# Optimization experiments

Measured on AMD Instinct MI355X. Metric: run time of the kernel, lower is better.

## Reference

```python
import jax, jax.numpy as jnp
import numpy as np

jax.config.update("jax_enable_x64", True)  # exact int64 fixed-point requantization

QMIN, QMAX = 0, 255  # 8-bit asymmetric activations


def _mul_m0_shift(acc, M0, shift):
    """gemmlowp-style fixed-point rescale: round((acc*M0)>>31) >> shift (rounding)."""
    prod = acc.astype(jnp.int64) * M0.astype(jnp.int64)
    nudge = jnp.where(prod >= 0, jnp.int64(1 << 30), jnp.int64(1 - (1 << 30)))
    hi = (prod + nudge) >> 31  # rounding-doubling high mul
    sh = shift.astype(jnp.int64)
    return (hi + (jnp.int64(1) << (sh - 1))) >> sh  # rounding right shift


def _requant(acc, M0, shift, z_out):
    return jnp.clip(_mul_m0_shift(acc, M0, shift) + z_out, QMIN, QMAX).astype(jnp.int32)


def _qconv(q, w, z_in, M0, shift, z_out, pad):
    # int8-style conv: subtract input zero-point, integer accumulate (exact in fp32
    # since |acc| < 2^24 by construction), then fixed-point requantize.
    xf = (q - z_in).astype(jnp.float32)
    acc = jax.lax.conv_general_dilated(
        xf, w, (1, 1), [(pad, pad), (pad, pad)],
        dimension_numbers=("NCHW", "OIHW", "NCHW"))
    return _requant(jnp.round(acc).astype(jnp.int64), M0, shift, z_out)


def _qbn(q, z_in, w, b, M0, shift, z_out):
    # fused quantized BN: per-channel integer affine + fixed-point requantize
    acc = (q.astype(jnp.int64) - z_in) * w.astype(jnp.int64)[None, :, None, None] \
          + b.astype(jnp.int64)[None, :, None, None]
    return _requant(acc, M0, shift, z_out)


def setup_inputs() -> dict:
    key = jax.random.key(0)
    ks = jax.random.split(key, 10)
    B, Cin, H, W = 32, 256, 56, 56
    width, Cout = 64, 256
    x = jax.random.randint(ks[0], (B, Cin, H, W), 0, 256, dtype=jnp.int32)
    w1 = jax.random.randint(ks[1], (width, Cin, 1, 1), -63, 64).astype(jnp.float32)
    w2 = jax.random.randint(ks[2], (width, width, 3, 3), -63, 64).astype(jnp.float32)
    w3 = jax.random.randint(ks[3], (Cout, width, 1, 1), -63, 64).astype(jnp.float32)
    bn1_w = jax.random.randint(ks[4], (width,), 100, 160).astype(jnp.float32)
    bn1_b = jax.random.randint(ks[5], (width,), -1000, 1000).astype(jnp.float32)
    bn2_w = jax.random.randint(ks[6], (width,), 100, 160).astype(jnp.float32)
    bn2_b = jax.random.randint(ks[7], (width,), -1000, 1000).astype(jnp.float32)
    bn3_w = jax.random.randint(ks[8], (Cout,), 100, 160).astype(jnp.float32)
    bn3_b = jax.random.randint(ks[9], (Cout,), -1000, 1000).astype(jnp.float32)
    conv_zin = jnp.array([128, 128, 128], jnp.int32)
    conv_m0 = jnp.array([1518500250] * 3, jnp.int32)
    conv_shift = jnp.array([9, 9, 9], jnp.int32)
    conv_zout = jnp.array([128, 128, 128], jnp.int32)
    bn_m0 = jnp.array([1073741824] * 3, jnp.int32)
    bn_shift = jnp.array([6, 6, 6], jnp.int32)
    bn_zout = jnp.array([128, 128, 128], jnp.int32)
    add_z = jnp.array([128, 128], jnp.int32)
    add_m0 = jnp.array([1073741824] * 2, jnp.int32)
    add_shift = jnp.array([1, 1], jnp.int32)
    add_zout = jnp.array(128, jnp.int32)
    return dict(x=x, w1=w1, w2=w2, w3=w3,
                bn1_w=bn1_w, bn1_b=bn1_b, bn2_w=bn2_w, bn2_b=bn2_b,
                bn3_w=bn3_w, bn3_b=bn3_b,
                conv_zin=conv_zin, conv_m0=conv_m0, conv_shift=conv_shift,
                conv_zout=conv_zout, bn_m0=bn_m0, bn_shift=bn_shift,
                bn_zout=bn_zout, add_z=add_z, add_m0=add_m0,
                add_shift=add_shift, add_zout=add_zout)


def reference(x, w1, w2, w3, bn1_w, bn1_b, bn2_w, bn2_b, bn3_w, bn3_b,
              conv_zin, conv_m0, conv_shift, conv_zout,
              bn_m0, bn_shift, bn_zout,
              add_z, add_m0, add_shift, add_zout):
    identity = x  # a_bit == target_bit -> rescale_matrix path skipped, conv_x = x
    out = _qconv(x, w1, conv_zin[0], conv_m0[0], conv_shift[0], conv_zout[0], 0)
    out = _qbn(out, conv_zout[0], bn1_w, bn1_b, bn_m0[0], bn_shift[0], bn_zout[0])
    out = _qconv(out, w2, conv_zin[1], conv_m0[1], conv_shift[1], conv_zout[1], 1)
    out = _qbn(out, conv_zout[1], bn2_w, bn2_b, bn_m0[1], bn_shift[1], bn_zout[1])
    out = _qconv(out, w3, conv_zin[2], conv_m0[2], conv_shift[2], conv_zout[2], 0)
    out = _qbn(out, conv_zout[2], bn3_w, bn3_b, bn_m0[2], bn_shift[2], bn_zout[2])
    # QuantizedAdd: rescale both branches to the output scale, add, clamp
    ra = _mul_m0_shift(identity.astype(jnp.int64) - add_z[0], add_m0[0], add_shift[0])
    rb = _mul_m0_shift(out.astype(jnp.int64) - add_z[1], add_m0[1], add_shift[1])
    return jnp.clip(ra + rb + add_zout, QMIN, QMAX).astype(jnp.int32)
```

## Files before the change

### kernel.cpp

```cpp
#include <hip/hip_runtime.h>


typedef int v4i __attribute__((ext_vector_type(4)));

#define BATCH 32
#define CIN 256
#define CMID 64
#define HW 3136
#define W56 56

#define T1_BYTES ((size_t)BATCH * HW * CMID)
#define WP_BYTES ((size_t)68 * 64 * 16)

__device__ __forceinline__ int requant_q(int acc, int M0, int shift, int zout) {
    long long prod = (long long)acc * (long long)M0;
    long long nudge = (prod >= 0) ? (1LL << 30) : (1LL - (1LL << 30));
    long long hi = (prod + nudge) >> 31;
    long long r = (hi + (1LL << (shift - 1))) >> shift;
    int v = (int)r + zout;
    return v < 0 ? 0 : (v > 255 ? 255 : v);
}

__device__ __forceinline__ long long mulshift_ll(long long v, int M0, int shift) {
    long long prod = v * (long long)M0;
    long long nudge = (prod >= 0) ? (1LL << 30) : (1LL - (1LL << 30));
    long long hi = (prod + nudge) >> 31;
    return (hi + (1LL << (shift - 1))) >> shift;
}

__device__ __forceinline__ v4i pack16f(const float* src, int stride) {
    v4i r;
#pragma unroll
    for (int d = 0; d < 4; ++d) {
        unsigned int u = 0;
#pragma unroll
        for (int by = 0; by < 4; ++by) {
            int v = (int)src[(d * 4 + by) * stride];
            u |= ((unsigned int)(v & 255)) << (8 * by);
        }
        r[d] = (int)u;
    }
    return r;
}

__global__ __launch_bounds__(256) void k_prep(
    const float* __restrict__ w1, const float* __restrict__ w2,
    const float* __restrict__ w3, v4i* __restrict__ wp)
{
    int id = blockIdx.x * 256 + threadIdx.x;
    int fid = id >> 6, lane = id & 63;
    if (fid >= 68) return;
    int col = lane & 15, ci0 = (lane >> 4) * 16;
    const float* src;
    int stride;
    if (fid < 16) {
        int wv = fid >> 2, ks = fid & 3;
        src = w1 + (size_t)(wv * 16 + col) * 256 + ks * 64 + ci0;
        stride = 1;
    } else if (fid < 52) {
        int i = fid - 16, wv = i / 9, t = i - wv * 9;
        src = w2 + ((size_t)(wv * 16 + col) * 64 + ci0) * 9 + t;
        stride = 9;
    } else {
        int s = fid - 52;
        src = w3 + (size_t)(s * 16 + col) * 64 + ci0;
        stride = 1;
    }
    wp[fid * 64 + lane] = pack16f(src, stride);
}

__global__ __launch_bounds__(256, 4) void k_conv1(
    const int* __restrict__ x, const v4i* __restrict__ wp1,
    const float* __restrict__ bn_w, const float* __restrict__ bn_b,
    const int* __restrict__ conv_zin, const int* __restrict__ conv_m0,
    const int* __restrict__ conv_shift, const int* __restrict__ conv_zout,
    const int* __restrict__ bn_m0, const int* __restrict__ bn_shift,
    const int* __restrict__ bn_zout, signed char* __restrict__ t1)
{
    __shared__ v4i sm[560];
    const int tid = threadIdx.x, lane = tid & 63, wv = tid >> 6;
    const int col = lane & 15, koff = lane >> 4;
    const int b = blockIdx.y;
    const int hw0 = blockIdx.x * 112;
    const int co0 = wv * 16;

    v4i a[4];
#pragma unroll
    for (int ks = 0; ks < 4; ++ks) a[ks] = wp1[(wv * 4 + ks) * 64 + lane];

    const int cg = tid & 7, q = tid >> 3;
    const bool act = q < 28;
    const int zin = conv_zin[0];
    const int* xbase = x + (size_t)b * CIN * HW + hw0 + 4 * q;

    v4i xa[8], xa2[8];
    if (act) {
#pragma unroll
        for (int j = 0; j < 8; ++j)
            xa[j] = *(const v4i*)(xbase + (size_t)(cg * 8 + j) * HW);
    }

    v4i acc[7];
#pragma unroll
    for (int i = 0; i < 7; ++i) acc[i] = (v4i){0, 0, 0, 0};

    unsigned long long* smu = (unsigned long long*)sm;
#pragma unroll
    for (int ks = 0; ks < 4; ++ks) {
        if (ks) __syncthreads();
        if (act) {
#pragma unroll
            for (int p = 0; p < 4; ++p) {
                unsigned int lo = 0, hi = 0;
#pragma unroll
                for (int j = 0; j < 4; ++j) {
                    lo |= ((unsigned int)((xa[j][p] - zin) & 255)) << (8 * j);
                    hi |= ((unsigned int)((xa[j + 4][p] - zin) & 255)) << (8 * j);
                }
                smu[(q * 4 + p) * 10 + cg] = ((unsigned long long)hi << 32) | lo;
            }
        }
        __syncthreads();
        if (ks < 3 && act) {
#pragma unroll
            for (int j = 0; j < 8; ++j)
                xa2[j] = *(const v4i*)(xbase + (size_t)((ks + 1) * 64 + cg * 8 + j) * HW);
        }
#pragma unroll
        for (int nt = 0; nt < 7; ++nt) {
            v4i bf = sm[(nt * 16 + col) * 5 + koff];
            acc[nt] = __builtin_amdgcn_mfma_i32_16x16x64_i8(a[ks], bf, acc[nt], 0, 0, 0);
        }
        if (ks < 3) {
#pragma unroll
            for (int j = 0; j < 8; ++j) xa[j] = xa2[j];
        }
    }

    const int cm0 = conv_m0[0], csh = conv_shift[0], czo = conv_zout[0];
    const int bm0 = bn_m0[0], bsh = bn_shift[0], bzo = bn_zout[0];
    const int zin2 = conv_zin[1];
    const int rowb = koff * 4;
    int bw[4], bb[4];
#pragma unroll
    for (int r = 0; r < 4; ++r) {
        bw[r] = (int)bn_w[co0 + rowb + r];
        bb[r] = (int)bn_b[co0 + rowb + r];
    }
#pragma unroll
    for (int nt = 0; nt < 7; ++nt) {
        int n = b * HW + hw0 + nt * 16 + col;
        unsigned int pkd = 0;
#pragma unroll
        for (int r = 0; r < 4; ++r) {
            int qv = requant_q(acc[nt][r], cm0, csh, czo);
            int a2 = (qv - czo) * bw[r] + bb[r];
            int q2 = requant_q(a2, bm0, bsh, bzo);
            pkd |= ((unsigned int)((q2 - zin2) & 255)) << (8 * r);
        }
        *(unsigned int*)(t1 + (size_t)n * 64 + co0 + rowb) = pkd;
    }
}

__global__ __launch_bounds__(256, 3) void k_conv23(
    const signed char* __restrict__ t1, const v4i* __restrict__ wp2,
    const v4i* __restrict__ wp3,
    const float* __restrict__ bn2_w, const float* __restrict__ bn2_b,
    const float* __restrict__ bn3_w, const float* __restrict__ bn3_b,
    const int* __restrict__ x,
    const int* __restrict__ conv_zin, const int* __restrict__ conv_m0,
    const int* __restrict__ conv_shift, const int* __restrict__ conv_zout,
    const int* __restrict__ bn_m0, const int* __restrict__ bn_shift,
    const int* __restrict__ bn_zout,
    const int* __restrict__ add_z, const int* __restrict__ add_m0,
    const int* __restrict__ add_shift, const int* __restrict__ add_zout,
    int* __restrict__ out)
{
    __shared__ v4i sm[1120];
    __shared__ v4i t2s[560];
    const int tid = threadIdx.x, lane = tid & 63, wv = tid >> 6;
    const int col = lane & 15, koff = lane >> 4;
    const int b = blockIdx.y;
    const int r0 = blockIdx.x * 2;
    const int co0 = wv * 16;
    const int rowb = koff * 4;

    v4i a[9];
#pragma unroll
    for (int t = 0; t < 9; ++t) a[t] = wp2[(wv * 9 + t) * 64 + lane];

    const v4i* t1v = (const v4i*)t1;
#pragma unroll
    for (int k = 0; k < 4; ++k) {
        int idx = tid + k * 256;
        if (idx < 896) {
            int pixl = idx >> 2, part = idx & 3;
            int lrow = pixl / W56, gw = pixl - lrow * W56;
            int grow = r0 - 1 + lrow;
            v4i v = (v4i){0, 0, 0, 0};
            if ((unsigned)grow < 56u)
                v = t1v[((size_t)b * HW + grow * W56 + gw) * 4 + part];
            sm[pixl * 5 + part] = v;
        }
    }
    __syncthreads();

    int orow[7], wc[7];
#pragma unroll
    for (int nt = 0; nt < 7; ++nt) {
        int pix = nt * 16 + col;
        orow[nt] = pix / W56;
        wc[nt] = pix - orow[nt] * W56;
    }

    v4i acc[7];
#pragma unroll
    for (int i = 0; i < 7; ++i) acc[i] = (v4i){0, 0, 0, 0};

#pragma unroll
    for (int kh = 0; kh < 3; ++kh) {
#pragma unroll
        for (int kw = 0; kw < 3; ++kw) {
            v4i af = a[kh * 3 + kw];
#pragma unroll
            for (int nt = 0; nt < 7; ++nt) {
                int sr = orow[nt] + kh;
                int sw = wc[nt] + kw - 1;
                bool valid = (unsigned)sw < 56u;
                v4i bf = sm[(sr * W56 + (valid ? sw : 0)) * 5 + koff];
                if (!valid) { bf[0] = 0; bf[1] = 0; bf[2] = 0; bf[3] = 0; }
                acc[nt] = __builtin_amdgcn_mfma_i32_16x16x64_i8(af, bf, acc[nt], 0, 0, 0);
            }
        }
    }

    {
        const int cm0 = conv_m0[1], csh = conv_shift[1], czo = conv_zout[1];
        const int bm0 = bn_m0[1], bsh = bn_shift[1], bzo = bn_zout[1];
        const int zin3 = conv_zin[2];
        int bw[4], bb[4];
#pragma unroll
        for (int r = 0; r < 4; ++r) {
            bw[r] = (int)bn2_w[co0 + rowb + r];
            bb[r] = (int)bn2_b[co0 + rowb + r];
        }
#pragma unroll
        for (int nt = 0; nt < 7; ++nt) {
            int pix = nt * 16 + col;
            unsigned int pkd = 0;
#pragma unroll
            for (int r = 0; r < 4; ++r) {
                int qv = requant_q(acc[nt][r], cm0, csh, czo);
                int a2 = (qv - czo) * bw[r] + bb[r];
                int q2 = requant_q(a2, bm0, bsh, bzo);
                pkd |= ((unsigned int)((q2 - zin3) & 255)) << (8 * r);
            }
            *(unsigned int*)((char*)t2s + (size_t)(pix * 5 + wv) * 16 + koff * 4) = pkd;
        }
    }
    __syncthreads();

    const int cm0 = conv_m0[2], csh = conv_shift[2], czo = conv_zout[2];
    const int bm0 = bn_m0[2], bsh = bn_shift[2], bzo = bn_zout[2];
    const int az0 = add_z[0], az1 = add_z[1];
    const int am0 = add_m0[0], am1 = add_m0[1];
    const int ash0 = add_shift[0], ash1 = add_shift[1];
    const int azout = add_zout[0];
    const int phw0 = r0 * W56;

#pragma unroll
    for (int s = 0; s < 4; ++s) {
        const int c0 = (wv * 4 + s) * 16;
        v4i a3 = wp3[(wv * 4 + s) * 64 + lane];

        int xv[7][4];
#pragma unroll
        for (int nt = 0; nt < 7; ++nt) {
            int phw = phw0 + nt * 16 + col;
#pragma unroll
            for (int r = 0; r < 4; ++r)
                xv[nt][r] = x[((size_t)b * CIN + c0 + rowb + r) * HW + phw];
        }

        v4i acc3[7];
#pragma unroll
        for (int i = 0; i < 7; ++i) acc3[i] = (v4i){0, 0, 0, 0};
#pragma unroll
        for (int nt = 0; nt < 7; ++nt) {
            v4i bf = t2s[(nt * 16 + col) * 5 + koff];
            acc3[nt] = __builtin_amdgcn_mfma_i32_16x16x64_i8(a3, bf, acc3[nt], 0, 0, 0);
        }

        int bw3[4], bb3[4];
#pragma unroll
        for (int r = 0; r < 4; ++r) {
            bw3[r] = (int)bn3_w[c0 + rowb + r];
            bb3[r] = (int)bn3_b[c0 + rowb + r];
        }
#pragma unroll
        for (int nt = 0; nt < 7; ++nt) {
            int phw = phw0 + nt * 16 + col;
#pragma unroll
            for (int r = 0; r < 4; ++r) {
                int qv = requant_q(acc3[nt][r], cm0, csh, czo);
                int a2 = (qv - czo) * bw3[r] + bb3[r];
                int q2 = requant_q(a2, bm0, bsh, bzo);
                long long ra = mulshift_ll((long long)(xv[nt][r] - az0), am0, ash0);
                long long rb = mulshift_ll((long long)(q2 - az1), am1, ash1);
                int res = (int)(ra + rb) + azout;
                res = res < 0 ? 0 : (res > 255 ? 255 : res);
                out[((size_t)b * CIN + c0 + rowb + r) * HW + phw] = res;
            }
        }
    }
}

extern "C" void kernel_launch(void* const* d_in, const int* in_sizes, int n_in,
                              void* d_out, int out_size, void* d_ws, size_t ws_size,
                              hipStream_t stream) {
    const int* x = (const int*)d_in[0];
    const float* w1 = (const float*)d_in[1];
    const float* w2 = (const float*)d_in[2];
    const float* w3 = (const float*)d_in[3];
    const float* bn1_w = (const float*)d_in[4];
    const float* bn1_b = (const float*)d_in[5];
    const float* bn2_w = (const float*)d_in[6];
    const float* bn2_b = (const float*)d_in[7];
    const float* bn3_w = (const float*)d_in[8];
    const float* bn3_b = (const float*)d_in[9];
    const int* conv_zin = (const int*)d_in[10];
    const int* conv_m0 = (const int*)d_in[11];
    const int* conv_shift = (const int*)d_in[12];
    const int* conv_zout = (const int*)d_in[13];
    const int* bn_m0 = (const int*)d_in[14];
    const int* bn_shift = (const int*)d_in[15];
    const int* bn_zout = (const int*)d_in[16];
    const int* add_z = (const int*)d_in[17];
    const int* add_m0 = (const int*)d_in[18];
    const int* add_shift = (const int*)d_in[19];
    const int* add_zout = (const int*)d_in[20];

    v4i* wp = (v4i*)d_ws;
    signed char* t1 = (signed char*)d_ws + WP_BYTES;

    const v4i* wp1 = wp;
    const v4i* wp2 = wp + 16 * 64;
    const v4i* wp3 = wp + 52 * 64;

    k_prep<<<dim3(17), dim3(256), 0, stream>>>(w1, w2, w3, wp);
    k_conv1<<<dim3(28, 32), dim3(256), 0, stream>>>(x, wp1, bn1_w, bn1_b,
        conv_zin, conv_m0, conv_shift, conv_zout, bn_m0, bn_shift, bn_zout, t1);
    k_conv23<<<dim3(28, 32), dim3(256), 0, stream>>>(t1, wp2, wp3,
        bn2_w, bn2_b, bn3_w, bn3_b, x,
        conv_zin, conv_m0, conv_shift, conv_zout, bn_m0, bn_shift, bn_zout,
        add_z, add_m0, add_shift, add_zout, (int*)d_out);
}
```

Baseline: 282.8 us.

## Shrink conv tiles, add weight-sum zero-point correction, simplify requant arithmetic

conv1 now works on 64-pixel tiles across 49 blocks per image. It packs input bytes with perm and XOR 0x80 and folds the input zero-point into the epilogue using precomputed per-channel weight sums. conv23 processes one output row per block with 4 tiles and prefetches the residual x values one step ahead. Requantization is folded into one 64-bit add and a high-word shift, and the pack uses perm instructions. Occupancy hints rise to 5 blocks per SIMD, which risks register pressure, and the one-row tiles waste 8 of 64 lanes in conv23.

```diff
diff --git a/kernel.cpp b/kernel.cpp
--- a/kernel.cpp
+++ b/kernel.cpp
@@ -9,23 +9,29 @@
 #define HW 3136
 #define W56 56
 
-#define T1_BYTES ((size_t)BATCH * HW * CMID)
 #define WP_BYTES ((size_t)68 * 64 * 16)
-
-__device__ __forceinline__ int requant_q(int acc, int M0, int shift, int zout) {
-    long long prod = (long long)acc * (long long)M0;
-    long long nudge = (prod >= 0) ? (1LL << 30) : (1LL - (1LL << 30));
-    long long hi = (prod + nudge) >> 31;
-    long long r = (hi + (1LL << (shift - 1))) >> shift;
-    int v = (int)r + zout;
+#define WSUM_BYTES ((size_t)64 * 4)
+
+__device__ __forceinline__ int rq_apply(int acc, int m0, long long cp, long long cn,
+                                        int shm1, int zo) {
+    long long prod = (long long)acc * m0;
+    prod += (prod >= 0) ? cp : cn;
+    int hi = (int)((unsigned long long)prod >> 32);
+    int v = (hi >> shm1) + zo;
     return v < 0 ? 0 : (v > 255 ? 255 : v);
 }
 
-__device__ __forceinline__ long long mulshift_ll(long long v, int M0, int shift) {
-    long long prod = v * (long long)M0;
-    long long nudge = (prod >= 0) ? (1LL << 30) : (1LL - (1LL << 30));
-    long long hi = (prod + nudge) >> 31;
-    return (hi + (1LL << (shift - 1))) >> shift;
+__device__ __forceinline__ int ms_apply(int xin, int m0, long long cp, long long cn,
+                                        int shm1) {
+    long long prod = (long long)xin * m0;
+    prod += (prod >= 0) ? cp : cn;
+    return ((int)((unsigned long long)prod >> 32)) >> shm1;
+}
+
+__device__ __forceinline__ unsigned int pk4x(int a0, int a1, int a2, int a3) {
+    unsigned p01 = __builtin_amdgcn_perm((unsigned)a1, (unsigned)a0, 0x00000400u);
+    unsigned p23 = __builtin_amdgcn_perm((unsigned)a3, (unsigned)a2, 0x04000000u);
+    return __builtin_amdgcn_perm(p23, p01, 0x07060100u);
 }
 
 __device__ __forceinline__ v4i pack16f(const float* src, int stride) {
@@ -45,124 +51,132 @@
 
 __global__ __launch_bounds__(256) void k_prep(
     const float* __restrict__ w1, const float* __restrict__ w2,
-    const float* __restrict__ w3, v4i* __restrict__ wp)
+    const float* __restrict__ w3, v4i* __restrict__ wp, int* __restrict__ wsum)
 {
-    int id = blockIdx.x * 256 + threadIdx.x;
-    int fid = id >> 6, lane = id & 63;
-    if (fid >= 68) return;
-    int col = lane & 15, ci0 = (lane >> 4) * 16;
-    const float* src;
-    int stride;
-    if (fid < 16) {
-        int wv = fid >> 2, ks = fid & 3;
-        src = w1 + (size_t)(wv * 16 + col) * 256 + ks * 64 + ci0;
-        stride = 1;
-    } else if (fid < 52) {
-        int i = fid - 16, wv = i / 9, t = i - wv * 9;
-        src = w2 + ((size_t)(wv * 16 + col) * 64 + ci0) * 9 + t;
-        stride = 9;
+    if (blockIdx.x < 17) {
+        int id = blockIdx.x * 256 + threadIdx.x;
+        int fid = id >> 6, lane = id & 63;
+        int col = lane & 15, ci0 = (lane >> 4) * 16;
+        const float* src;
+        int stride;
+        if (fid < 16) {
+            int wv = fid >> 2, ks = fid & 3;
+            src = w1 + (size_t)(wv * 16 + col) * 256 + ks * 64 + ci0;
+            stride = 1;
+        } else if (fid < 52) {
+            int i = fid - 16, wv = i / 9, t = i - wv * 9;
+            src = w2 + ((size_t)(wv * 16 + col) * 64 + ci0) * 9 + t;
+            stride = 9;
+        } else {
+            int s = fid - 52;
+            src = w3 + (size_t)(s * 16 + col) * 64 + ci0;
+            stride = 1;
+        }
+        wp[fid * 64 + lane] = pack16f(src, stride);
     } else {
-        int s = fid - 52;
-        src = w3 + (size_t)(s * 16 + col) * 64 + ci0;
-        stride = 1;
-    }
-    wp[fid * 64 + lane] = pack16f(src, stride);
-}
-
-__global__ __launch_bounds__(256, 4) void k_conv1(
+        int ch = threadIdx.x >> 2, t4 = threadIdx.x & 3;
+        int s = 0;
+        for (int i = 0; i < 64; ++i) s += (int)w1[(size_t)ch * 256 + t4 * 64 + i];
+        s += __shfl_xor(s, 1);
+        s += __shfl_xor(s, 2);
+        if (t4 == 0) wsum[ch] = s;
+    }
+}
+
+__global__ __launch_bounds__(256, 5) void k_conv1(
     const int* __restrict__ x, const v4i* __restrict__ wp1,
+    const int* __restrict__ wsum1,
     const float* __restrict__ bn_w, const float* __restrict__ bn_b,
     const int* __restrict__ conv_zin, const int* __restrict__ conv_m0,
     const int* __restrict__ conv_shift, const int* __restrict__ conv_zout,
     const int* __restrict__ bn_m0, const int* __restrict__ bn_shift,
     const int* __restrict__ bn_zout, signed char* __restrict__ t1)
 {
-    __shared__ v4i sm[560];
+    __shared__ v4i sm[320];
     const int tid = threadIdx.x, lane = tid & 63, wv = tid >> 6;
     const int col = lane & 15, koff = lane >> 4;
     const int b = blockIdx.y;
-    const int hw0 = blockIdx.x * 112;
+    const int hw0 = blockIdx.x * 64;
     const int co0 = wv * 16;
 
     v4i a[4];
 #pragma unroll
     for (int ks = 0; ks < 4; ++ks) a[ks] = wp1[(wv * 4 + ks) * 64 + lane];
 
-    const int cg = tid & 7, q = tid >> 3;
-    const bool act = q < 28;
-    const int zin = conv_zin[0];
+    const int cg = tid & 15, q = tid >> 4;
     const int* xbase = x + (size_t)b * CIN * HW + hw0 + 4 * q;
 
-    v4i xa[8], xa2[8];
-    if (act) {
-#pragma unroll
-        for (int j = 0; j < 8; ++j)
-            xa[j] = *(const v4i*)(xbase + (size_t)(cg * 8 + j) * HW);
-    }
-
-    v4i acc[7];
-#pragma unroll
-    for (int i = 0; i < 7; ++i) acc[i] = (v4i){0, 0, 0, 0};
-
-    unsigned long long* smu = (unsigned long long*)sm;
+    v4i xa[4], xa2[4];
+#pragma unroll
+    for (int j = 0; j < 4; ++j)
+        xa[j] = *(const v4i*)(xbase + (size_t)(cg * 4 + j) * HW);
+
+    v4i acc[4];
+#pragma unroll
+    for (int i = 0; i < 4; ++i) acc[i] = (v4i){0, 0, 0, 0};
+
+    unsigned* smx = (unsigned*)sm;
 #pragma unroll
     for (int ks = 0; ks < 4; ++ks) {
         if (ks) __syncthreads();
-        if (act) {
-#pragma unroll
-            for (int p = 0; p < 4; ++p) {
-                unsigned int lo = 0, hi = 0;
-#pragma unroll
-                for (int j = 0; j < 4; ++j) {
-                    lo |= ((unsigned int)((xa[j][p] - zin) & 255)) << (8 * j);
-                    hi |= ((unsigned int)((xa[j + 4][p] - zin) & 255)) << (8 * j);
-                }
-                smu[(q * 4 + p) * 10 + cg] = ((unsigned long long)hi << 32) | lo;
-            }
+#pragma unroll
+        for (int p = 0; p < 4; ++p) {
+            unsigned pkd = pk4x(xa[0][p], xa[1][p], xa[2][p], xa[3][p]) ^ 0x80808080u;
+            smx[(q * 4 + p) * 20 + cg] = pkd;
         }
         __syncthreads();
-        if (ks < 3 && act) {
-#pragma unroll
-            for (int j = 0; j < 8; ++j)
-                xa2[j] = *(const v4i*)(xbase + (size_t)((ks + 1) * 64 + cg * 8 + j) * HW);
-        }
-#pragma unroll
-        for (int nt = 0; nt < 7; ++nt) {
+        if (ks < 3) {
+#pragma unroll
+            for (int j = 0; j < 4; ++j)
+                xa2[j] = *(const v4i*)(xbase + (size_t)((ks + 1) * 64 + cg * 4 + j) * HW);
+        }
+#pragma unroll
+        for (int nt = 0; nt < 4; ++nt) {
             v4i bf = sm[(nt * 16 + col) * 5 + koff];
             acc[nt] = __builtin_amdgcn_mfma_i32_16x16x64_i8(a[ks], bf, acc[nt], 0, 0, 0);
         }
         if (ks < 3) {
 #pragma unroll
-            for (int j = 0; j < 8; ++j) xa[j] = xa2[j];
-        }
-    }
-
+            for (int j = 0; j < 4; ++j) xa[j] = xa2[j];
+        }
+    }
+
+    const int zin = conv_zin[0];
+    const int corr0 = 128 - zin;
     const int cm0 = conv_m0[0], csh = conv_shift[0], czo = conv_zout[0];
     const int bm0 = bn_m0[0], bsh = bn_shift[0], bzo = bn_zout[0];
     const int zin2 = conv_zin[1];
+    const long long cbv = 1LL << (30 + csh);
+    const long long ccp = cbv + (1LL << 30), ccn = cbv + 1 - (1LL << 30);
+    const int cshm1 = csh - 1;
+    const long long bbv = 1LL << (30 + bsh);
+    const long long bcp = bbv + (1LL << 30), bcn = bbv + 1 - (1LL << 30);
+    const int bshm1 = bsh - 1;
     const int rowb = koff * 4;
-    int bw[4], bb[4];
+    int bw[4], bbx[4], ws[4];
 #pragma unroll
     for (int r = 0; r < 4; ++r) {
         bw[r] = (int)bn_w[co0 + rowb + r];
-        bb[r] = (int)bn_b[co0 + rowb + r];
-    }
-#pragma unroll
-    for (int nt = 0; nt < 7; ++nt) {
+        bbx[r] = (int)bn_b[co0 + rowb + r] - czo * bw[r];
+        ws[r] = wsum1[co0 + rowb + r];
+    }
+#pragma unroll
+    for (int nt = 0; nt < 4; ++nt) {
         int n = b * HW + hw0 + nt * 16 + col;
-        unsigned int pkd = 0;
+        int e[4];
 #pragma unroll
         for (int r = 0; r < 4; ++r) {
-            int qv = requant_q(acc[nt][r], cm0, csh, czo);
-            int a2 = (qv - czo) * bw[r] + bb[r];
-            int q2 = requant_q(a2, bm0, bsh, bzo);
-            pkd |= ((unsigned int)((q2 - zin2) & 255)) << (8 * r);
-        }
-        *(unsigned int*)(t1 + (size_t)n * 64 + co0 + rowb) = pkd;
-    }
-}
-
-__global__ __launch_bounds__(256, 3) void k_conv23(
+            int av = acc[nt][r] + corr0 * ws[r];
+            int qv = rq_apply(av, cm0, ccp, ccn, cshm1, czo);
+            int a2 = qv * bw[r] + bbx[r];
+            int q2 = rq_apply(a2, bm0, bcp, bcn, bshm1, bzo);
+            e[r] = q2 - zin2;
+        }
+        *(unsigned*)(t1 + (size_t)n * 64 + co0 + rowb) = pk4x(e[0], e[1], e[2], e[3]);
+    }
+}
+
+__global__ __launch_bounds__(256, 5) void k_conv23(
     const signed char* __restrict__ t1, const v4i* __restrict__ wp2,
     const v4i* __restrict__ wp3,
     const float* __restrict__ bn2_w, const float* __restrict__ bn2_b,
@@ -176,14 +190,13 @@
     const int* __restrict__ add_shift, const int* __restrict__ add_zout,
     int* __restrict__ out)
 {
-    __shared__ v4i sm[1120];
-    __shared__ v4i t2s[560];
+    __shared__ v4i sm[840];
+    __shared__ v4i t2s[320];
     const int tid = threadIdx.x, lane = tid & 63, wv = tid >> 6;
     const int col = lane & 15, koff = lane >> 4;
     const int b = blockIdx.y;
-    const int r0 = blockIdx.x * 2;
-    const int co0 = wv * 16;
-    const int rowb = koff * 4;
+    const int r0 = blockIdx.x;
+    const int co0 = wv * 16, rowb = koff * 4;
 
     v4i a[9];
 #pragma unroll
@@ -191,9 +204,9 @@
 
     const v4i* t1v = (const v4i*)t1;
 #pragma unroll
-    for (int k = 0; k < 4; ++k) {
+    for (int k = 0; k < 3; ++k) {
         int idx = tid + k * 256;
-        if (idx < 896) {
+        if (idx < 672) {
             int pixl = idx >> 2, part = idx & 3;
             int lrow = pixl / W56, gw = pixl - lrow * W56;
             int grow = r0 - 1 + lrow;
@@ -205,17 +218,9 @@
     }
     __syncthreads();
 
-    int orow[7], wc[7];
-#pragma unroll
-    for (int nt = 0; nt < 7; ++nt) {
-        int pix = nt * 16 + col;
-        orow[nt] = pix / W56;
-        wc[nt] = pix - orow[nt] * W56;
-    }
-
-    v4i acc[7];
-#pragma unroll
-    for (int i = 0; i < 7; ++i) acc[i] = (v4i){0, 0, 0, 0};
+    v4i acc[4];
+#pragma unroll
+    for (int i = 0; i < 4; ++i) acc[i] = (v4i){0, 0, 0, 0};
 
 #pragma unroll
     for (int kh = 0; kh < 3; ++kh) {
@@ -223,94 +228,135 @@
         for (int kw = 0; kw < 3; ++kw) {
             v4i af = a[kh * 3 + kw];
 #pragma unroll
-            for (int nt = 0; nt < 7; ++nt) {
-                int sr = orow[nt] + kh;
-                int sw = wc[nt] + kw - 1;
+            for (int nt = 0; nt < 4; ++nt) {
+                int sw = nt * 16 + col + kw - 1;
                 bool valid = (unsigned)sw < 56u;
-                v4i bf = sm[(sr * W56 + (valid ? sw : 0)) * 5 + koff];
+                v4i bf = sm[(kh * W56 + (valid ? sw : 0)) * 5 + koff];
                 if (!valid) { bf[0] = 0; bf[1] = 0; bf[2] = 0; bf[3] = 0; }
                 acc[nt] = __builtin_amdgcn_mfma_i32_16x16x64_i8(af, bf, acc[nt], 0, 0, 0);
             }
         }
     }
+
+    v4i a3x[4];
+#pragma unroll
+    for (int s = 0; s < 4; ++s) a3x[s] = wp3[(wv * 4 + s) * 64 + lane];
+
+    int pxc[4];
+#pragma unroll
+    for (int nt = 0; nt < 4; ++nt) {
+        int px = nt * 16 + col;
+        pxc[nt] = px < 56 ? px : 55;
+    }
+    const size_t xoff = (size_t)b * CIN * HW + (size_t)rowb * HW + r0 * W56;
+    const int* xb = x + xoff;
+    int* ob = out + xoff;
+
+    int xv[4][4];
+#pragma unroll
+    for (int nt = 0; nt < 4; ++nt)
+#pragma unroll
+        for (int r = 0; r < 4; ++r)
+            xv[nt][r] = xb[(size_t)(wv * 64 + r) * HW + pxc[nt]];
 
     {
         const int cm0 = conv_m0[1], csh = conv_shift[1], czo = conv_zout[1];
         const int bm0 = bn_m0[1], bsh = bn_shift[1], bzo = bn_zout[1];
         const int zin3 = conv_zin[2];
-        int bw[4], bb[4];
+        const long long cbv = 1LL << (30 + csh);
+        const long long ccp = cbv + (1LL << 30), ccn = cbv + 1 - (1LL << 30);
+        const int cshm1 = csh - 1;
+        const long long bbv = 1LL << (30 + bsh);
+        const long long bcp = bbv + (1LL << 30), bcn = bbv + 1 - (1LL << 30);
+        const int bshm1 = bsh - 1;
+        int bw[4], bbx[4];
 #pragma unroll
         for (int r = 0; r < 4; ++r) {
             bw[r] = (int)bn2_w[co0 + rowb + r];
-            bb[r] = (int)bn2_b[co0 + rowb + r];
-        }
-#pragma unroll
-        for (int nt = 0; nt < 7; ++nt) {
+            bbx[r] = (int)bn2_b[co0 + rowb + r] - czo * bw[r];
+        }
+#pragma unroll
+        for (int nt = 0; nt < 4; ++nt) {
             int pix = nt * 16 + col;
-            unsigned int pkd = 0;
+            int e[4];
 #pragma unroll
             for (int r = 0; r < 4; ++r) {
-                int qv = requant_q(acc[nt][r], cm0, csh, czo);
-                int a2 = (qv - czo) * bw[r] + bb[r];
-                int q2 = requant_q(a2, bm0, bsh, bzo);
-                pkd |= ((unsigned int)((q2 - zin3) & 255)) << (8 * r);
+                int qv = rq_apply(acc[nt][r], cm0, ccp, ccn, cshm1, czo);
+                int a2 = qv * bw[r] + bbx[r];
+                int q2 = rq_apply(a2, bm0, bcp, bcn, bshm1, bzo);
+                e[r] = q2 - zin3;
             }
-            *(unsigned int*)((char*)t2s + (size_t)(pix * 5 + wv) * 16 + koff * 4) = pkd;
+            *(unsigned*)((char*)t2s + (size_t)(pix * 5 + wv) * 16 + koff * 4) =
+                pk4x(e[0], e[1], e[2], e[3]);
         }
     }
     __syncthreads();
 
     const int cm0 = conv_m0[2], csh = conv_shift[2], czo = conv_zout[2];
     const int bm0 = bn_m0[2], bsh = bn_shift[2], bzo = bn_zout[2];
+    const long long cb3 = 1LL << (30 + csh);
+    const long long ccp = cb3 + (1LL << 30), ccn = cb3 + 1 - (1LL << 30);
+    const int cshm1 = csh - 1;
+    const long long bb3 = 1LL << (30 + bsh);
+    const long long bcp = bb3 + (1LL << 30), bcn = bb3 + 1 - (1LL << 30);
+    const int bshm1 = bsh - 1;
     const int az0 = add_z[0], az1 = add_z[1];
     const int am0 = add_m0[0], am1 = add_m0[1];
     const int ash0 = add_shift[0], ash1 = add_shift[1];
+    const long long a0b = 1LL << (30 + ash0);
+    const long long acp0 = a0b + (1LL << 30), acn0 = a0b + 1 - (1LL << 30);
+    const int ashm0 = ash0 - 1;
+    const long long a1b = 1LL << (30 + ash1);
+    const long long acp1 = a1b + (1LL << 30), acn1 = a1b + 1 - (1LL << 30);
+    const int ashm1 = ash1 - 1;
     const int azout = add_zout[0];
-    const int phw0 = r0 * W56;
 
 #pragma unroll
     for (int s = 0; s < 4; ++s) {
-        const int c0 = (wv * 4 + s) * 16;
-        v4i a3 = wp3[(wv * 4 + s) * 64 + lane];
-
-        int xv[7][4];
-#pragma unroll
-        for (int nt = 0; nt < 7; ++nt) {
-            int phw = phw0 + nt * 16 + col;
-#pragma unroll
-            for (int r = 0; r < 4; ++r)
-                xv[nt][r] = x[((size_t)b * CIN + c0 + rowb + r) * HW + phw];
-        }
-
-        v4i acc3[7];
-#pragma unroll
-        for (int i = 0; i < 7; ++i) acc3[i] = (v4i){0, 0, 0, 0};
-#pragma unroll
-        for (int nt = 0; nt < 7; ++nt) {
+        const int c0 = wv * 64 + s * 16;
+        int xn[4][4];
+        if (s < 3) {
+#pragma unroll
+            for (int nt = 0; nt < 4; ++nt)
+#pragma unroll
+                for (int r = 0; r < 4; ++r)
+                    xn[nt][r] = xb[(size_t)(c0 + 16 + r) * HW + pxc[nt]];
+        }
+        v4i acc3[4];
+#pragma unroll
+        for (int i = 0; i < 4; ++i) acc3[i] = (v4i){0, 0, 0, 0};
+#pragma unroll
+        for (int nt = 0; nt < 4; ++nt) {
             v4i bf = t2s[(nt * 16 + col) * 5 + koff];
-            acc3[nt] = __builtin_amdgcn_mfma_i32_16x16x64_i8(a3, bf, acc3[nt], 0, 0, 0);
-        }
-
-        int bw3[4], bb3[4];
+            acc3[nt] = __builtin_amdgcn_mfma_i32_16x16x64_i8(a3x[s], bf, acc3[nt], 0, 0, 0);
+        }
+        int bw3[4], bbx3[4];
 #pragma unroll
         for (int r = 0; r < 4; ++r) {
             bw3[r] = (int)bn3_w[c0 + rowb + r];
-            bb3[r] = (int)bn3_b[c0 + rowb + r];
-        }
-#pragma unroll
-        for (int nt = 0; nt < 7; ++nt) {
-            int phw = phw0 + nt * 16 + col;
+            bbx3[r] = (int)bn3_b[c0 + rowb + r] - czo * bw3[r];
+        }
+#pragma unroll
+        for (int nt = 0; nt < 4; ++nt) {
+            bool st = (nt * 16 + col) < 56;
 #pragma unroll
             for (int r = 0; r < 4; ++r) {
-                int qv = requant_q(acc3[nt][r], cm0, csh, czo);
-                int a2 = (qv - czo) * bw3[r] + bb3[r];
-                int q2 = requant_q(a2, bm0, bsh, bzo);
-                long long ra = mulshift_ll((long long)(xv[nt][r] - az0), am0, ash0);
-                long long rb = mulshift_ll((long long)(q2 - az1), am1, ash1);
-                int res = (int)(ra + rb) + azout;
+                int qv = rq_apply(acc3[nt][r], cm0, ccp, ccn, cshm1, czo);
+                int a2 = qv * bw3[r] + bbx3[r];
+                int q2 = rq_apply(a2, bm0, bcp, bcn, bshm1, bzo);
+                int ra = ms_apply(xv[nt][r] - az0, am0, acp0, acn0, ashm0);
+                int rb = ms_apply(q2 - az1, am1, acp1, acn1, ashm1);
+                int res = ra + rb + azout;
                 res = res < 0 ? 0 : (res > 255 ? 255 : res);
-                out[((size_t)b * CIN + c0 + rowb + r) * HW + phw] = res;
+                if (st) ob[(size_t)(c0 + r) * HW + pxc[nt]] = res;
             }
+        }
+        if (s < 3) {
+#pragma unroll
+            for (int nt = 0; nt < 4; ++nt)
+#pragma unroll
+                for (int r = 0; r < 4; ++r)
+                    xv[nt][r] = xn[nt][r];
         }
     }
 }
@@ -341,16 +387,17 @@
     const int* add_zout = (const int*)d_in[20];
 
     v4i* wp = (v4i*)d_ws;
-    signed char* t1 = (signed char*)d_ws + WP_BYTES;
+    int* wsum1 = (int*)((char*)d_ws + WP_BYTES);
+    signed char* t1 = (signed char*)d_ws + WP_BYTES + WSUM_BYTES;
 
     const v4i* wp1 = wp;
     const v4i* wp2 = wp + 16 * 64;
     const v4i* wp3 = wp + 52 * 64;
 
-    k_prep<<<dim3(17), dim3(256), 0, stream>>>(w1, w2, w3, wp);
-    k_conv1<<<dim3(28, 32), dim3(256), 0, stream>>>(x, wp1, bn1_w, bn1_b,
+    k_prep<<<dim3(18), dim3(256), 0, stream>>>(w1, w2, w3, wp, wsum1);
+    k_conv1<<<dim3(49, 32), dim3(256), 0, stream>>>(x, wp1, wsum1, bn1_w, bn1_b,
         conv_zin, conv_m0, conv_shift, conv_zout, bn_m0, bn_shift, bn_zout, t1);
-    k_conv23<<<dim3(28, 32), dim3(256), 0, stream>>>(t1, wp2, wp3,
+    k_conv23<<<dim3(56, 32), dim3(256), 0, stream>>>(t1, wp2, wp3,
         bn2_w, bn2_b, bn3_w, bn3_b, x,
         conv_zin, conv_m0, conv_shift, conv_zout, bn_m0, bn_shift, bn_zout,
         add_z, add_m0, add_shift, add_zout, (int*)d_out);
```

Result: slower. 307.0 us (+8.5%).
